# Optimization experiments

Hardware: AMD Instinct MI355X
Metric: run time of the kernel (lower is better)

Reference implementation:

```python
import jax, jax.numpy as jnp
import numpy as np

B, D, H = 1024, 128, 128
LN_EPS = 1e-5


def setup_inputs() -> dict:
    key = jax.random.key(0)
    ks = jax.random.split(key, 12)
    s_d = 1.0 / np.sqrt(D)
    s_h = 1.0 / np.sqrt(H)
    return {
        "x": jax.random.normal(ks[0], (B, D), dtype=jnp.float32),
        # diff_proj: Linear(D, H)
        "Wd": jax.random.uniform(ks[1], (H, D), jnp.float32, -s_d, s_d),
        "bd": jax.random.uniform(ks[2], (H,), jnp.float32, -s_d, s_d),
        # tau_proj: Linear(D, 1) -> Softplus
        "Wt": jax.random.uniform(ks[3], (1, D), jnp.float32, -s_d, s_d),
        "bt": jax.random.uniform(ks[4], (1,), jnp.float32, -s_d, s_d),
        # agg: Linear(H, H) -> ReLU
        "Wa": jax.random.uniform(ks[5], (H, H), jnp.float32, -s_h, s_h),
        "ba": jax.random.uniform(ks[6], (H,), jnp.float32, -s_h, s_h),
        # res_proj: Linear(D, H)
        "Wr": jax.random.uniform(ks[7], (H, D), jnp.float32, -s_d, s_d),
        "br": jax.random.uniform(ks[8], (H,), jnp.float32, -s_d, s_d),
        # LayerNorm(H)
        "gamma": jnp.ones((H,), jnp.float32),
        "beta": jnp.zeros((H,), jnp.float32),
    }


def reference(x, Wd, bd, Wt, bt, Wa, ba, Wr, br, gamma, beta):
    # mean_j diff_proj(|x_i - x_j|) == diff_proj(mean_j |x_i - x_j|) since Linear is affine
    diffs_mean = jnp.mean(jnp.abs(x[:, None, :] - x[None, :, :]), axis=1)  # [B, D]
    d_mean = diffs_mean @ Wd.T + bd                                         # [B, H]
    # tau = softplus(x Wt^T + bt).clamp(min=0.01) + 1.0
    tau = jnp.clip(jax.nn.softplus(x @ Wt.T + bt), 0.01, None) + 1.0        # [B, 1]
    h_mean = d_mean / tau
    h = jax.nn.relu(h_mean @ Wa.T + ba)
    y = h + x @ Wr.T + br
    mu = jnp.mean(y, axis=-1, keepdims=True)
    var = jnp.var(y, axis=-1, keepdims=True)
    return (y - mu) / jnp.sqrt(var + LN_EPS) * gamma + beta
```

## Files before the change

### kernel.cpp

```cpp
#include <hip/hip_runtime.h>
#include <math.h>

#define Bn 1024
#define Dn 128
#define Hn 128

__global__ __launch_bounds__(1024) void fused_resd1(
    const float* __restrict__ x,
    const float* __restrict__ Wd, const float* __restrict__ bd,
    const float* __restrict__ Wt, const float* __restrict__ bt,
    const float* __restrict__ Wa, const float* __restrict__ ba,
    const float* __restrict__ Wr, const float* __restrict__ br,
    const float* __restrict__ gamma, const float* __restrict__ beta,
    float* __restrict__ out) {
  const int t = threadIdx.x;
  const int c = t & 31;
  const int g = t >> 5;
  const int i0 = blockIdx.x << 2;

  __shared__ float red[32][4][Dn];
  __shared__ float xs[4][Dn];
  __shared__ float dms[4][Dn];
  __shared__ float ms[4][Hn];
  __shared__ float ys[4][Hn];
  __shared__ float wt_s[Dn];
  __shared__ float tau_s[4];

  float4 xi[4];
#pragma unroll
  for (int r = 0; r < 4; ++r)
    xi[r] = *(const float4*)(x + (size_t)(i0 + r) * Dn + c * 4);

  float4 acc[4];
#pragma unroll
  for (int r = 0; r < 4; ++r) acc[r] = make_float4(0.f, 0.f, 0.f, 0.f);

  const float4* xq = (const float4*)x + (size_t)g * 32 * (Dn / 4) + c;
#pragma unroll 1
  for (int jj = 0; jj < 32; jj += 4) {
    float4 xj[4];
#pragma unroll
    for (int u = 0; u < 4; ++u) xj[u] = xq[(size_t)(jj + u) * (Dn / 4)];
#pragma unroll
    for (int u = 0; u < 4; ++u) {
#pragma unroll
      for (int r = 0; r < 4; ++r) {
        acc[r].x += fabsf(xi[r].x - xj[u].x);
        acc[r].y += fabsf(xi[r].y - xj[u].y);
        acc[r].z += fabsf(xi[r].z - xj[u].z);
        acc[r].w += fabsf(xi[r].w - xj[u].w);
      }
    }
  }
#pragma unroll
  for (int r = 0; r < 4; ++r) *(float4*)&red[g][r][c * 4] = acc[r];
  __syncthreads();

  if (t < 512) {
    const int r = t >> 7, d = t & 127;
    float s = 0.f;
#pragma unroll
    for (int gg = 0; gg < 32; ++gg) s += red[gg][r][d];
    dms[r][d] = s * (1.0f / 1024.0f);
    xs[r][d] = x[(size_t)(i0 + r) * Dn + d];
  } else if (t < 640) {
    wt_s[t - 512] = Wt[t - 512];
  }
  __syncthreads();

  if (t < 256) {
    const int r = t >> 6, p = t & 63;
    float partial = xs[r][p] * wt_s[p] + xs[r][p + 64] * wt_s[p + 64];
#pragma unroll
    for (int off = 32; off; off >>= 1) partial += __shfl_xor(partial, off, 64);
    if (p == 0) {
      const float z = partial + bt[0];
      const float sp = fmaxf(z, 0.f) + log1pf(expf(-fabsf(z)));
      tau_s[r] = 1.0f / (fmaxf(sp, 0.01f) + 1.0f);
    }
  }
  __syncthreads();

  if (t < 256) {
    const int h = t & 127;
    const int g4 = t >> 7;
    const int r0 = 2 * g4, r1 = 2 * g4 + 1;
    float m0 = bd[h], m1 = m0;
    const float4* w = (const float4*)(Wd + (size_t)h * Dn);
#pragma unroll 4
    for (int k4 = 0; k4 < Dn / 4; ++k4) {
      const float4 wv = w[k4];
      const int k = k4 * 4;
      m0 += wv.x * dms[r0][k] + wv.y * dms[r0][k + 1] + wv.z * dms[r0][k + 2] + wv.w * dms[r0][k + 3];
      m1 += wv.x * dms[r1][k] + wv.y * dms[r1][k + 1] + wv.z * dms[r1][k + 2] + wv.w * dms[r1][k + 3];
    }
    ms[r0][h] = m0 * tau_s[r0];
    ms[r1][h] = m1 * tau_s[r1];
  }
  __syncthreads();

  if (t < 256) {
    const int h = t & 127;
    const int g4 = t >> 7;
    const int r0 = 2 * g4, r1 = 2 * g4 + 1;
    float q0 = ba[h], q1 = q0, c0 = br[h], c1 = c0;
    const float4* wa = (const float4*)(Wa + (size_t)h * Dn);
    const float4* wr = (const float4*)(Wr + (size_t)h * Dn);
#pragma unroll 4
    for (int k4 = 0; k4 < Dn / 4; ++k4) {
      const float4 av = wa[k4];
      const float4 rv = wr[k4];
      const int k = k4 * 4;
      q0 += av.x * ms[r0][k] + av.y * ms[r0][k + 1] + av.z * ms[r0][k + 2] + av.w * ms[r0][k + 3];
      q1 += av.x * ms[r1][k] + av.y * ms[r1][k + 1] + av.z * ms[r1][k + 2] + av.w * ms[r1][k + 3];
      c0 += rv.x * xs[r0][k] + rv.y * xs[r0][k + 1] + rv.z * xs[r0][k + 2] + rv.w * xs[r0][k + 3];
      c1 += rv.x * xs[r1][k] + rv.y * xs[r1][k + 1] + rv.z * xs[r1][k + 2] + rv.w * xs[r1][k + 3];
    }
    ys[r0][h] = fmaxf(q0, 0.f) + c0;
    ys[r1][h] = fmaxf(q1, 0.f) + c1;
  }
  __syncthreads();

  if (t < 256) {
    const int r = t >> 6, p = t & 63;
    const float v0 = ys[r][p], v1 = ys[r][p + 64];
    float s = v0 + v1;
    float q = v0 * v0 + v1 * v1;
#pragma unroll
    for (int off = 32; off; off >>= 1) {
      s += __shfl_xor(s, off, 64);
      q += __shfl_xor(q, off, 64);
    }
    const float mu = s * (1.0f / 128.0f);
    const float var = q * (1.0f / 128.0f) - mu * mu;
    const float rs = rsqrtf(var + 1e-5f);
    float* o = out + (size_t)(i0 + r) * Hn;
    o[p]      = (v0 - mu) * rs * gamma[p]      + beta[p];
    o[p + 64] = (v1 - mu) * rs * gamma[p + 64] + beta[p + 64];
  }
}

extern "C" void kernel_launch(void* const* d_in, const int* in_sizes, int n_in,
                              void* d_out, int out_size, void* d_ws, size_t ws_size,
                              hipStream_t stream) {
  const float* x     = (const float*)d_in[0];
  const float* Wd    = (const float*)d_in[1];
  const float* bd    = (const float*)d_in[2];
  const float* Wt    = (const float*)d_in[3];
  const float* bt    = (const float*)d_in[4];
  const float* Wa    = (const float*)d_in[5];
  const float* ba    = (const float*)d_in[6];
  const float* Wr    = (const float*)d_in[7];
  const float* br    = (const float*)d_in[8];
  const float* gamma = (const float*)d_in[9];
  const float* beta  = (const float*)d_in[10];
  float* out = (float*)d_out;

  fused_resd1<<<Bn / 4, 1024, 0, stream>>>(x, Wd, bd, Wt, bt, Wa, ba, Wr, br,
                                           gamma, beta, out);
  (void)in_sizes; (void)n_in; (void)out_size; (void)d_ws; (void)ws_size;
}
```

Before: 96.46 us.

## Split fused kernel into pairwise-reduction and epilogue kernels with j-split grid

Splits the single 1024-thread kernel into two launches. The first computes partial pairwise |xi-xj| sums over a 2D grid (256 row tiles × 8 column chunks) with 256-thread blocks and writes the partials to workspace. The second reduces those partials and runs the projection, tau, aggregation and LayerNorm epilogue with all 256 threads active. This raises occupancy and the number of blocks, and removes the idle threads from the epilogue, at the cost of a second launch and a workspace round trip through global memory.

New measurement: 99.78 us. +3.4%, slower.

```diff
diff --git a/kernel.cpp b/kernel.cpp
--- a/kernel.cpp
+++ b/kernel.cpp
@@ -5,26 +5,15 @@
 #define Dn 128
 #define Hn 128
 
-__global__ __launch_bounds__(1024) void fused_resd1(
-    const float* __restrict__ x,
-    const float* __restrict__ Wd, const float* __restrict__ bd,
-    const float* __restrict__ Wt, const float* __restrict__ bt,
-    const float* __restrict__ Wa, const float* __restrict__ ba,
-    const float* __restrict__ Wr, const float* __restrict__ br,
-    const float* __restrict__ gamma, const float* __restrict__ beta,
-    float* __restrict__ out) {
+__global__ __launch_bounds__(256, 8) void k1_pairs(
+    const float* __restrict__ x, float* __restrict__ ws) {
   const int t = threadIdx.x;
   const int c = t & 31;
-  const int g = t >> 5;
+  const int q = t >> 5;
   const int i0 = blockIdx.x << 2;
+  const int jb = (blockIdx.y << 7) + (q << 4);
 
-  __shared__ float red[32][4][Dn];
-  __shared__ float xs[4][Dn];
-  __shared__ float dms[4][Dn];
-  __shared__ float ms[4][Hn];
-  __shared__ float ys[4][Hn];
-  __shared__ float wt_s[Dn];
-  __shared__ float tau_s[4];
+  __shared__ float red[8][4][Dn];
 
   float4 xi[4];
 #pragma unroll
@@ -35,40 +24,72 @@
 #pragma unroll
   for (int r = 0; r < 4; ++r) acc[r] = make_float4(0.f, 0.f, 0.f, 0.f);
 
-  const float4* xq = (const float4*)x + (size_t)g * 32 * (Dn / 4) + c;
+  const float4* xq = (const float4*)x + (size_t)jb * (Dn / 4) + c;
 #pragma unroll 1
-  for (int jj = 0; jj < 32; jj += 4) {
-    float4 xj[4];
+  for (int j = 0; j < 16; j += 2) {
+    const float4 xj0 = xq[(size_t)j * (Dn / 4)];
+    const float4 xj1 = xq[(size_t)(j + 1) * (Dn / 4)];
 #pragma unroll
-    for (int u = 0; u < 4; ++u) xj[u] = xq[(size_t)(jj + u) * (Dn / 4)];
+    for (int r = 0; r < 4; ++r) {
+      acc[r].x += fabsf(xi[r].x - xj0.x);
+      acc[r].y += fabsf(xi[r].y - xj0.y);
+      acc[r].z += fabsf(xi[r].z - xj0.z);
+      acc[r].w += fabsf(xi[r].w - xj0.w);
+    }
 #pragma unroll
-    for (int u = 0; u < 4; ++u) {
-#pragma unroll
-      for (int r = 0; r < 4; ++r) {
-        acc[r].x += fabsf(xi[r].x - xj[u].x);
-        acc[r].y += fabsf(xi[r].y - xj[u].y);
-        acc[r].z += fabsf(xi[r].z - xj[u].z);
-        acc[r].w += fabsf(xi[r].w - xj[u].w);
-      }
+    for (int r = 0; r < 4; ++r) {
+      acc[r].x += fabsf(xi[r].x - xj1.x);
+      acc[r].y += fabsf(xi[r].y - xj1.y);
+      acc[r].z += fabsf(xi[r].z - xj1.z);
+      acc[r].w += fabsf(xi[r].w - xj1.w);
     }
   }
 #pragma unroll
-  for (int r = 0; r < 4; ++r) *(float4*)&red[g][r][c * 4] = acc[r];
+  for (int r = 0; r < 4; ++r) *(float4*)&red[q][r][c * 4] = acc[r];
   __syncthreads();
 
-  if (t < 512) {
-    const int r = t >> 7, d = t & 127;
-    float s = 0.f;
+  float* wsp = ws + ((size_t)(blockIdx.x << 3) + blockIdx.y) * 512;
 #pragma unroll
-    for (int gg = 0; gg < 32; ++gg) s += red[gg][r][d];
-    dms[r][d] = s * (1.0f / 1024.0f);
-    xs[r][d] = x[(size_t)(i0 + r) * Dn + d];
-  } else if (t < 640) {
-    wt_s[t - 512] = Wt[t - 512];
+  for (int s = t; s < 512; s += 256) {
+    float v = 0.f;
+#pragma unroll
+    for (int qq = 0; qq < 8; ++qq) v += red[qq][s >> 7][s & 127];
+    wsp[s] = v;
   }
+}
+
+__global__ __launch_bounds__(256) void k2_epilogue(
+    const float* __restrict__ x, const float* __restrict__ ws,
+    const float* __restrict__ Wd, const float* __restrict__ bd,
+    const float* __restrict__ Wt, const float* __restrict__ bt,
+    const float* __restrict__ Wa, const float* __restrict__ ba,
+    const float* __restrict__ Wr, const float* __restrict__ br,
+    const float* __restrict__ gamma, const float* __restrict__ beta,
+    float* __restrict__ out) {
+  const int t = threadIdx.x;
+  const int itile = blockIdx.x;
+  const int i0 = itile << 2;
+
+  __shared__ float xs[4][Dn];
+  __shared__ float dms[4][Dn];
+  __shared__ float ms[4][Hn];
+  __shared__ float ys[4][Hn];
+  __shared__ float wt_s[Dn];
+  __shared__ float tau_s[4];
+
+  const float* wsp = ws + (size_t)(itile << 3) * 512;
+#pragma unroll
+  for (int s = t; s < 512; s += 256) {
+    float v = 0.f;
+#pragma unroll
+    for (int js = 0; js < 8; ++js) v += wsp[js * 512 + s];
+    dms[s >> 7][s & 127] = v * (1.0f / 1024.0f);
+    xs[s >> 7][s & 127] = x[((size_t)itile << 9) + s];
+  }
+  if (t < 128) wt_s[t] = Wt[t];
   __syncthreads();
 
-  if (t < 256) {
+  {
     const int r = t >> 6, p = t & 63;
     float partial = xs[r][p] * wt_s[p] + xs[r][p + 64] * wt_s[p + 64];
 #pragma unroll
@@ -81,10 +102,10 @@
   }
   __syncthreads();
 
-  if (t < 256) {
-    const int h = t & 127;
-    const int g4 = t >> 7;
-    const int r0 = 2 * g4, r1 = 2 * g4 + 1;
+  const int h = t & 127;
+  const int g4 = t >> 7;
+  const int r0 = 2 * g4, r1 = 2 * g4 + 1;
+  {
     float m0 = bd[h], m1 = m0;
     const float4* w = (const float4*)(Wd + (size_t)h * Dn);
 #pragma unroll 4
@@ -99,10 +120,7 @@
   }
   __syncthreads();
 
-  if (t < 256) {
-    const int h = t & 127;
-    const int g4 = t >> 7;
-    const int r0 = 2 * g4, r1 = 2 * g4 + 1;
+  {
     float q0 = ba[h], q1 = q0, c0 = br[h], c1 = c0;
     const float4* wa = (const float4*)(Wa + (size_t)h * Dn);
     const float4* wr = (const float4*)(Wr + (size_t)h * Dn);
@@ -121,18 +139,18 @@
   }
   __syncthreads();
 
-  if (t < 256) {
+  {
     const int r = t >> 6, p = t & 63;
     const float v0 = ys[r][p], v1 = ys[r][p + 64];
     float s = v0 + v1;
-    float q = v0 * v0 + v1 * v1;
+    float qq = v0 * v0 + v1 * v1;
 #pragma unroll
     for (int off = 32; off; off >>= 1) {
       s += __shfl_xor(s, off, 64);
-      q += __shfl_xor(q, off, 64);
+      qq += __shfl_xor(qq, off, 64);
     }
     const float mu = s * (1.0f / 128.0f);
-    const float var = q * (1.0f / 128.0f) - mu * mu;
+    const float var = qq * (1.0f / 128.0f) - mu * mu;
     const float rs = rsqrtf(var + 1e-5f);
     float* o = out + (size_t)(i0 + r) * Hn;
     o[p]      = (v0 - mu) * rs * gamma[p]      + beta[p];
@@ -155,8 +173,11 @@
   const float* gamma = (const float*)d_in[9];
   const float* beta  = (const float*)d_in[10];
   float* out = (float*)d_out;
+  float* ws = (float*)d_ws;
 
-  fused_resd1<<<Bn / 4, 1024, 0, stream>>>(x, Wd, bd, Wt, bt, Wa, ba, Wr, br,
-                                           gamma, beta, out);
-  (void)in_sizes; (void)n_in; (void)out_size; (void)d_ws; (void)ws_size;
+  dim3 g1(Bn / 4, 8);
+  k1_pairs<<<g1, 256, 0, stream>>>(x, ws);
+  k2_epilogue<<<Bn / 4, 256, 0, stream>>>(x, ws, Wd, bd, Wt, bt, Wa, ba,
+                                          Wr, br, gamma, beta, out);
+  (void)in_sizes; (void)n_in; (void)out_size; (void)ws_size;
 }
```

## Stage x tiles through double-buffered shared memory with register prefetch

Applied to the files above, without the earlier changes.

The all-pairs absolute-difference loop no longer has each thread read its j rows straight from global memory. Threads now cooperatively copy 128-row chunks of x into two 64KB shared-memory buffers. The next chunk is prefetched into registers while the current one is consumed, so global load latency can overlap with compute. The cost is a much larger manual shared-memory carve-out (about 137KB, with the reduction array aliased onto buffer 0), an extra LDS write and read per element, and a block-wide barrier per chunk.

Result: slower. 121.4 us (+25.8%).

```diff
diff --git a/kernel.cpp b/kernel.cpp
--- a/kernel.cpp
+++ b/kernel.cpp
@@ -14,55 +14,80 @@
     const float* __restrict__ gamma, const float* __restrict__ beta,
     float* __restrict__ out) {
   const int t = threadIdx.x;
-  const int c = t & 31;
-  const int g = t >> 5;
+  const int c4 = t & 31;
+  const int q = t >> 5;
   const int i0 = blockIdx.x << 2;
 
-  __shared__ float red[32][4][Dn];
-  __shared__ float xs[4][Dn];
-  __shared__ float dms[4][Dn];
-  __shared__ float ms[4][Hn];
-  __shared__ float ys[4][Hn];
-  __shared__ float wt_s[Dn];
-  __shared__ float tau_s[4];
+  __shared__ __align__(16) unsigned char smem_raw[139792];
+  float* const sbuf0 = (float*)smem_raw;
+  float* const sbuf1 = (float*)(smem_raw + 65536);
+  float* const red   = (float*)smem_raw;
+  float* const xs    = (float*)(smem_raw + 131072);
+  float* const dms   = xs + 512;
+  float* const ms    = dms + 512;
+  float* const ys    = ms + 512;
+  float* const wt_s  = ys + 512;
+  float* const tau_s = wt_s + 128;
 
   float4 xi[4];
 #pragma unroll
   for (int r = 0; r < 4; ++r)
-    xi[r] = *(const float4*)(x + (size_t)(i0 + r) * Dn + c * 4);
+    xi[r] = *(const float4*)(x + (size_t)(i0 + r) * Dn + c4 * 4);
 
   float4 acc[4];
 #pragma unroll
   for (int r = 0; r < 4; ++r) acc[r] = make_float4(0.f, 0.f, 0.f, 0.f);
 
-  const float4* xq = (const float4*)x + (size_t)g * 32 * (Dn / 4) + c;
+  const float4* gx = (const float4*)x;
+
+  {
+    float4 s0[4];
+#pragma unroll
+    for (int u = 0; u < 4; ++u) s0[u] = gx[u * 1024 + t];
+#pragma unroll
+    for (int u = 0; u < 4; ++u) *(float4*)(sbuf0 + (u * 1024 + t) * 4) = s0[u];
+  }
+
 #pragma unroll 1
-  for (int jj = 0; jj < 32; jj += 4) {
-    float4 xj[4];
+  for (int k = 0; k < 8; ++k) {
+    float4 nx[4];
+    if (k < 7) {
 #pragma unroll
-    for (int u = 0; u < 4; ++u) xj[u] = xq[(size_t)(jj + u) * (Dn / 4)];
+      for (int u = 0; u < 4; ++u)
+        nx[u] = gx[(size_t)(k + 1) * 4096 + u * 1024 + t];
+    }
+    __syncthreads();
+    const float* tbp = ((k & 1) ? sbuf1 : sbuf0) + (q * 4) * Dn + c4 * 4;
 #pragma unroll
     for (int u = 0; u < 4; ++u) {
+      const float4 xj = *(const float4*)(tbp + u * Dn);
 #pragma unroll
       for (int r = 0; r < 4; ++r) {
-        acc[r].x += fabsf(xi[r].x - xj[u].x);
-        acc[r].y += fabsf(xi[r].y - xj[u].y);
-        acc[r].z += fabsf(xi[r].z - xj[u].z);
-        acc[r].w += fabsf(xi[r].w - xj[u].w);
+        acc[r].x += fabsf(xi[r].x - xj.x);
+        acc[r].y += fabsf(xi[r].y - xj.y);
+        acc[r].z += fabsf(xi[r].z - xj.z);
+        acc[r].w += fabsf(xi[r].w - xj.w);
       }
     }
+    if (k < 7) {
+      float* nb = ((k + 1) & 1) ? sbuf1 : sbuf0;
+#pragma unroll
+      for (int u = 0; u < 4; ++u) *(float4*)(nb + (u * 1024 + t) * 4) = nx[u];
+    }
   }
+
 #pragma unroll
-  for (int r = 0; r < 4; ++r) *(float4*)&red[g][r][c * 4] = acc[r];
+  for (int r = 0; r < 4; ++r)
+    *(float4*)(red + q * 512 + r * Dn + c4 * 4) = acc[r];
   __syncthreads();
 
   if (t < 512) {
     const int r = t >> 7, d = t & 127;
     float s = 0.f;
 #pragma unroll
-    for (int gg = 0; gg < 32; ++gg) s += red[gg][r][d];
-    dms[r][d] = s * (1.0f / 1024.0f);
-    xs[r][d] = x[(size_t)(i0 + r) * Dn + d];
+    for (int qq = 0; qq < 32; ++qq) s += red[qq * 512 + r * Dn + d];
+    dms[r * Dn + d] = s * (1.0f / 1024.0f);
+    xs[r * Dn + d] = x[(size_t)(i0 + r) * Dn + d];
   } else if (t < 640) {
     wt_s[t - 512] = Wt[t - 512];
   }
@@ -70,7 +95,7 @@
 
   if (t < 256) {
     const int r = t >> 6, p = t & 63;
-    float partial = xs[r][p] * wt_s[p] + xs[r][p + 64] * wt_s[p + 64];
+    float partial = xs[r * Dn + p] * wt_s[p] + xs[r * Dn + p + 64] * wt_s[p + 64];
 #pragma unroll
     for (int off = 32; off; off >>= 1) partial += __shfl_xor(partial, off, 64);
     if (p == 0) {
@@ -91,11 +116,13 @@
     for (int k4 = 0; k4 < Dn / 4; ++k4) {
       const float4 wv = w[k4];
       const int k = k4 * 4;
-      m0 += wv.x * dms[r0][k] + wv.y * dms[r0][k + 1] + wv.z * dms[r0][k + 2] + wv.w * dms[r0][k + 3];
-      m1 += wv.x * dms[r1][k] + wv.y * dms[r1][k + 1] + wv.z * dms[r1][k + 2] + wv.w * dms[r1][k + 3];
+      m0 += wv.x * dms[r0 * Dn + k] + wv.y * dms[r0 * Dn + k + 1] +
+            wv.z * dms[r0 * Dn + k + 2] + wv.w * dms[r0 * Dn + k + 3];
+      m1 += wv.x * dms[r1 * Dn + k] + wv.y * dms[r1 * Dn + k + 1] +
+            wv.z * dms[r1 * Dn + k + 2] + wv.w * dms[r1 * Dn + k + 3];
     }
-    ms[r0][h] = m0 * tau_s[r0];
-    ms[r1][h] = m1 * tau_s[r1];
+    ms[r0 * Dn + h] = m0 * tau_s[r0];
+    ms[r1 * Dn + h] = m1 * tau_s[r1];
   }
   __syncthreads();
 
@@ -111,28 +138,32 @@
       const float4 av = wa[k4];
       const float4 rv = wr[k4];
       const int k = k4 * 4;
-      q0 += av.x * ms[r0][k] + av.y * ms[r0][k + 1] + av.z * ms[r0][k + 2] + av.w * ms[r0][k + 3];
-      q1 += av.x * ms[r1][k] + av.y * ms[r1][k + 1] + av.z * ms[r1][k + 2] + av.w * ms[r1][k + 3];
-      c0 += rv.x * xs[r0][k] + rv.y * xs[r0][k + 1] + rv.z * xs[r0][k + 2] + rv.w * xs[r0][k + 3];
-      c1 += rv.x * xs[r1][k] + rv.y * xs[r1][k + 1] + rv.z * xs[r1][k + 2] + rv.w * xs[r1][k + 3];
+      q0 += av.x * ms[r0 * Dn + k] + av.y * ms[r0 * Dn + k + 1] +
+            av.z * ms[r0 * Dn + k + 2] + av.w * ms[r0 * Dn + k + 3];
+      q1 += av.x * ms[r1 * Dn + k] + av.y * ms[r1 * Dn + k + 1] +
+            av.z * ms[r1 * Dn + k + 2] + av.w * ms[r1 * Dn + k + 3];
+      c0 += rv.x * xs[r0 * Dn + k] + rv.y * xs[r0 * Dn + k + 1] +
+            rv.z * xs[r0 * Dn + k + 2] + rv.w * xs[r0 * Dn + k + 3];
+      c1 += rv.x * xs[r1 * Dn + k] + rv.y * xs[r1 * Dn + k + 1] +
+            rv.z * xs[r1 * Dn + k + 2] + rv.w * xs[r1 * Dn + k + 3];
     }
-    ys[r0][h] = fmaxf(q0, 0.f) + c0;
-    ys[r1][h] = fmaxf(q1, 0.f) + c1;
+    ys[r0 * Dn + h] = fmaxf(q0, 0.f) + c0;
+    ys[r1 * Dn + h] = fmaxf(q1, 0.f) + c1;
   }
   __syncthreads();
 
   if (t < 256) {
     const int r = t >> 6, p = t & 63;
-    const float v0 = ys[r][p], v1 = ys[r][p + 64];
+    const float v0 = ys[r * Dn + p], v1 = ys[r * Dn + p + 64];
     float s = v0 + v1;
-    float q = v0 * v0 + v1 * v1;
+    float qq = v0 * v0 + v1 * v1;
 #pragma unroll
     for (int off = 32; off; off >>= 1) {
       s += __shfl_xor(s, off, 64);
-      q += __shfl_xor(q, off, 64);
+      qq += __shfl_xor(qq, off, 64);
     }
     const float mu = s * (1.0f / 128.0f);
-    const float var = q * (1.0f / 128.0f) - mu * mu;
+    const float var = qq * (1.0f / 128.0f) - mu * mu;
     const float rs = rsqrtf(var + 1e-5f);
     float* o = out + (size_t)(i0 + r) * Hn;
     o[p]      = (v0 - mu) * rs * gamma[p]      + beta[p];
```
